# Optimization experiments

Measured on AMD Instinct MI355X. Metric: run time of the kernel, lower is better.

The kernel has to match this reference:

```python
import jax, jax.numpy as jnp
import numpy as np

N, C, H, W = 8, 128, 128, 128   # batch, emb channels, spatial
O, M, K, L = 81, 1, 3, 3        # classes, num_modes, neg_num_modes, neg MPC layers
SIGMA, BETA, NEG_SCOPE = 0.5, 0.3, 2.0
EPS = 1e-12


def _l2norm(v, axis):
    # matches F.normalize: v / max(||v||, eps)
    n = jnp.sqrt(jnp.sum(v * v, axis=axis, keepdims=True))
    return v / jnp.maximum(n, EPS)


def setup_inputs() -> dict:
    key = jax.random.key(0)
    k0, k1, k2 = jax.random.split(key, 3)
    return {
        "x": jax.random.normal(k0, (N, C, H, W), jnp.float32),
        "rep_fc_w": jax.random.normal(k1, (O * M * C,), jnp.float32) * 0.01,
        "rep_fc_b": jnp.zeros((O * M * C,), jnp.float32),
        "neg_w": jax.random.normal(k2, (K, L, C, C), jnp.float32) * 0.01,
        "neg_b": jnp.zeros((K, L, C), jnp.float32),
    }


def reference(x, rep_fc_w, rep_fc_b, neg_w, neg_b):
    # emb_module = identity; L2-normalize embeddings over channel dim
    e = _l2norm(x, axis=1)                      # (N,C,H,W)
    ehw = e.transpose(0, 2, 3, 1)               # (N,H,W,C)

    # reps = rep_fc(1.0) -> weight + bias (Linear(1, O*M*C) applied to scalar 1)
    reps = (rep_fc_w + rep_fc_b).reshape(O, M, C)
    reps = _l2norm(reps, axis=2)                # (O,1,C) unit rows

    # negative reps: K independent 3-layer MLPs (ReLU between layers)
    r = reps[:, 0, :]                           # (O,C)
    neg_list = []
    for k in range(K):
        h = r
        for l in range(L):
            h = h @ neg_w[k, l].T + neg_b[k, l]
            if l < L - 1:
                h = jax.nn.relu(h)
        neg_list.append(h)
    reps_neg = jnp.stack(neg_list, axis=1)      # (O,K,C)
    reps_neg = _l2norm(reps_neg, axis=2)

    # Both sides unit-norm -> ||e - r||^2 = 2 - 2<e,r>; compute via GEMM
    dot = jnp.einsum('nhwc,omc->nomhw', ehw, reps)        # (N,O,M,H,W)
    distances = jnp.sqrt(jax.nn.relu(2.0 - 2.0 * dot))
    dot_n = jnp.einsum('nhwc,okc->nokhw', ehw, reps_neg)  # (N,O,K,H,W)
    distances_neg = jnp.sqrt(jax.nn.relu(2.0 - 2.0 * dot_n))

    inv = 1.0 / (2.0 * SIGMA ** 2)
    probs_neg = jnp.exp(-distances_neg ** 2 * inv)
    cls_score_neg = probs_neg.max(axis=2)                 # (N,O,H,W)

    probs_ori = jnp.exp(-distances ** 2 * inv).max(axis=2)  # (N,O,H,W)

    min_neg = distances_neg.min(axis=2, keepdims=True)    # (N,O,1,H,W)
    probs = jnp.exp(-(distances + BETA * jax.nn.relu(NEG_SCOPE - min_neg)) ** 2 * inv)

    # cls_norm = True: normalize summed probs over classes
    probs_sumj = probs.sum(axis=2)                        # (N,O,H,W)
    cls_score = probs_sumj / probs_sumj.sum(axis=1, keepdims=True)

    return (cls_score, cls_score_neg, distances, distances_neg, probs_ori)
```

## Files before the change

kernel.cpp:

```cpp
#include <hip/hip_runtime.h>

#define HW 16384

typedef __attribute__((ext_vector_type(8))) short bf16x8;
typedef __attribute__((ext_vector_type(4))) float f32x4;

static constexpr size_t OFF0 = 0;
static constexpr size_t OFF1 = 10616832;
static constexpr size_t OFF2 = 21233664;
static constexpr size_t OFF3 = 31850496;
static constexpr size_t OFF4 = 63700992;

static constexpr size_t WS_R    = 0;
static constexpr size_t WS_H1   = 41472;
static constexpr size_t WS_H2   = 165888;
static constexpr size_t WS_NEGN = 290304;
static constexpr size_t WS_A    = 414720;

static __device__ __forceinline__ unsigned short f2bf(float f) {
  unsigned int u = __float_as_uint(f);
  u += 0x7fffu + ((u >> 16) & 1u);
  return (unsigned short)(u >> 16);
}

__global__ __launch_bounds__(128) void prep_first(const float* __restrict__ rw,
                                                  const float* __restrict__ rb,
                                                  const float* __restrict__ nw,
                                                  const float* __restrict__ nb,
                                                  float* __restrict__ ws_r,
                                                  float* __restrict__ ws_out) {
  const int b = blockIdx.x;
  const int k = b / 81, o = b % 81;
  const int j = threadIdx.x;
  __shared__ float hrow[128];
  __shared__ float red[2];

  float v = rw[o * 128 + j] + rb[o * 128 + j];
  float sq = v * v;
#pragma unroll
  for (int m = 1; m < 64; m <<= 1) sq += __shfl_xor(sq, m, 64);
  if ((j & 63) == 0) red[j >> 6] = sq;
  __syncthreads();
  float tot = red[0] + red[1];
  float r = v / fmaxf(sqrtf(tot), 1e-12f);
  if (k == 0) ws_r[o * 128 + j] = r;
  hrow[j] = r;
  __syncthreads();

  const float4* Wr = (const float4*)(nw + (((size_t)(k * 3 + 0)) * 128 + j) * 128);
  const float4* H  = (const float4*)hrow;
  float4 a = {0.f, 0.f, 0.f, 0.f};
#pragma unroll
  for (int q = 0; q < 32; ++q) {
    float4 wv = Wr[q]; float4 hv = H[q];
    a.x = fmaf(wv.x, hv.x, a.x); a.y = fmaf(wv.y, hv.y, a.y);
    a.z = fmaf(wv.z, hv.z, a.z); a.w = fmaf(wv.w, hv.w, a.w);
  }
  float acc = (a.x + a.y) + (a.z + a.w);
  acc += nb[(k * 3 + 0) * 128 + j];
  acc = fmaxf(acc, 0.f);
  ws_out[((size_t)(k * 81 + o)) * 128 + j] = acc;
}

__global__ __launch_bounds__(128) void prep_stage(const float* __restrict__ in,
                                                  const float* __restrict__ nw,
                                                  const float* __restrict__ nb,
                                                  float* __restrict__ out,
                                                  int l, int do_relu, int do_norm) {
  const int b = blockIdx.x;
  const int k = b / 81, o = b % 81;
  const int j = threadIdx.x;
  __shared__ float hrow[128];
  __shared__ float red[2];

  hrow[j] = in[((size_t)(k * 81 + o)) * 128 + j];
  __syncthreads();

  const float4* Wr = (const float4*)(nw + (((size_t)(k * 3 + l)) * 128 + j) * 128);
  const float4* H  = (const float4*)hrow;
  float4 a = {0.f, 0.f, 0.f, 0.f};
#pragma unroll
  for (int q = 0; q < 32; ++q) {
    float4 wv = Wr[q]; float4 hv = H[q];
    a.x = fmaf(wv.x, hv.x, a.x); a.y = fmaf(wv.y, hv.y, a.y);
    a.z = fmaf(wv.z, hv.z, a.z); a.w = fmaf(wv.w, hv.w, a.w);
  }
  float acc = (a.x + a.y) + (a.z + a.w);
  acc += nb[(k * 3 + l) * 128 + j];
  if (do_relu) acc = fmaxf(acc, 0.f);
  if (do_norm) {
    float sq = acc * acc;
#pragma unroll
    for (int m = 1; m < 64; m <<= 1) sq += __shfl_xor(sq, m, 64);
    if ((j & 63) == 0) red[j >> 6] = sq;
    __syncthreads();
    float tot = red[0] + red[1];
    acc = acc / fmaxf(sqrtf(tot), 1e-12f);
  }
  out[((size_t)(k * 81 + o)) * 128 + j] = acc;
}

__global__ __launch_bounds__(64) void prep_pack(const float* __restrict__ ws_r,
                                                const float* __restrict__ ws_negn,
                                                bf16x8* __restrict__ wsA) {
  const int mt = blockIdx.x >> 2, ks = blockIdx.x & 3;
  const int l = threadIdx.x;
  const int row = mt * 16 + (l & 15);
  const int o = row >> 2, s = row & 3;
  const int k0 = ks * 32 + (l >> 4) * 8;
  bf16x8 r = {0, 0, 0, 0, 0, 0, 0, 0};
  if (o < 81) {
    const float* src = (s == 0) ? (ws_r + (size_t)o * 128)
                                : (ws_negn + ((size_t)((s - 1) * 81 + o)) * 128);
#pragma unroll
    for (int jj = 0; jj < 8; ++jj) r[jj] = (short)f2bf(src[k0 + jj]);
  }
  wsA[(mt * 4 + ks) * 64 + l] = r;
}

__global__ __launch_bounds__(256) void main_kernel(const float* __restrict__ x,
                                                   const bf16x8* __restrict__ wsA,
                                                   float* __restrict__ out) {
  __shared__ __align__(16) char eLds[32768];
  __shared__ float ss[8][128];
  __shared__ float invn[128];

  const int b = blockIdx.x;
  const int n = b >> 7;
  const int p0 = (b & 127) << 7;
  const int t = threadIdx.x;
  const float* xb = x + ((size_t)n * 128) * HW + p0;

  {
    const int pq = (t & 31) * 4;
    const int cg = t >> 5;
    float a0 = 0.f, a1 = 0.f, a2 = 0.f, a3 = 0.f;
#pragma unroll
    for (int i = 0; i < 16; ++i) {
      const int c = i * 8 + cg;
      float4 v = *(const float4*)(xb + (size_t)c * HW + pq);
      a0 = fmaf(v.x, v.x, a0); a1 = fmaf(v.y, v.y, a1);
      a2 = fmaf(v.z, v.z, a2); a3 = fmaf(v.w, v.w, a3);
      const int c2 = c * 2;
      *(unsigned short*)(eLds + (((pq + 0) * 256 + c2) ^ (((pq + 0) & 7) << 4))) = f2bf(v.x);
      *(unsigned short*)(eLds + (((pq + 1) * 256 + c2) ^ (((pq + 1) & 7) << 4))) = f2bf(v.y);
      *(unsigned short*)(eLds + (((pq + 2) * 256 + c2) ^ (((pq + 2) & 7) << 4))) = f2bf(v.z);
      *(unsigned short*)(eLds + (((pq + 3) * 256 + c2) ^ (((pq + 3) & 7) << 4))) = f2bf(v.w);
    }
    float4 st = {a0, a1, a2, a3};
    *(float4*)&ss[cg][pq] = st;
  }
  __syncthreads();
  if (t < 128) {
    float s = 0.f;
#pragma unroll
    for (int g = 0; g < 8; ++g) s += ss[g][t];
    invn[t] = 1.f / fmaxf(sqrtf(s), 1e-12f);
  }
  __syncthreads();

  const int lane = t & 63;
  const int wv = t >> 6;
  const int og = lane >> 4;

  bf16x8 bfrag[2][4];
  float ivp[2];
#pragma unroll
  for (int u = 0; u < 2; ++u) {
    const int p = (wv * 2 + u) * 16 + (lane & 15);
#pragma unroll
    for (int ks = 0; ks < 4; ++ks) {
      const int addr = (p * 256 + ks * 64 + (lane >> 4) * 16) ^ ((p & 7) << 4);
      bfrag[u][ks] = *(const bf16x8*)(eLds + addr);
    }
    ivp[u] = invn[p];
  }

  float probs_arr[42];

#pragma unroll
  for (int mt = 0; mt < 21; ++mt) {
    bf16x8 afr[4];
#pragma unroll
    for (int ks = 0; ks < 4; ++ks) afr[ks] = wsA[(mt * 4 + ks) * 64 + lane];
    f32x4 c0 = {0.f, 0.f, 0.f, 0.f}, c1 = {0.f, 0.f, 0.f, 0.f};
#pragma unroll
    for (int ks = 0; ks < 4; ++ks) {
      c0 = __builtin_amdgcn_mfma_f32_16x16x32_bf16(afr[ks], bfrag[0][ks], c0, 0, 0, 0);
      c1 = __builtin_amdgcn_mfma_f32_16x16x32_bf16(afr[ks], bfrag[1][ks], c1, 0, 0, 0);
    }
    const int o = mt * 4 + og;
    const bool valid = (o < 81);
#pragma unroll
    for (int u = 0; u < 2; ++u) {
      const f32x4 c = u ? c1 : c0;
      const float iv = ivp[u];
      float q0 = fmaxf(2.f - 2.f * (c[0] * iv), 0.f);
      float d0 = sqrtf(q0);
      float d1 = sqrtf(fmaxf(2.f - 2.f * (c[1] * iv), 0.f));
      float d2 = sqrtf(fmaxf(2.f - 2.f * (c[2] * iv), 0.f));
      float d3 = sqrtf(fmaxf(2.f - 2.f * (c[3] * iv), 0.f));
      float dmin = fminf(d1, fminf(d2, d3));
      float pneg = __expf(-2.f * dmin * dmin);
      float pori = __expf(-2.f * q0);
      float tt = d0 + 0.3f * fmaxf(2.f - dmin, 0.f);
      float pr = __expf(-2.f * tt * tt);
      probs_arr[mt * 2 + u] = valid ? pr : 0.f;
      if (valid) {
        const int pimg = p0 + (wv * 2 + u) * 16 + (lane & 15);
        const size_t base = ((size_t)(n * 81 + o)) * HW + pimg;
        out[OFF2 + base] = d0;
        out[OFF4 + base] = pori;
        out[OFF1 + base] = pneg;
        const size_t b3 = ((size_t)((n * 81 + o) * 3)) * HW + pimg;
        out[OFF3 + b3] = d1;
        out[OFF3 + b3 + HW] = d2;
        out[OFF3 + b3 + 2 * HW] = d3;
      }
    }
  }

#pragma unroll
  for (int u = 0; u < 2; ++u) {
    float s = 0.f;
#pragma unroll
    for (int mt = 0; mt < 21; ++mt) s += probs_arr[mt * 2 + u];
    s += __shfl_xor(s, 16, 64);
    s += __shfl_xor(s, 32, 64);
    const float is = 1.f / s;
    const int pimg = p0 + (wv * 2 + u) * 16 + (lane & 15);
#pragma unroll
    for (int mt = 0; mt < 21; ++mt) {
      const int o = mt * 4 + og;
      if (o < 81) {
        const size_t base = ((size_t)(n * 81 + o)) * HW + pimg;
        out[OFF0 + base] = probs_arr[mt * 2 + u] * is;
      }
    }
  }
}

extern "C" void kernel_launch(void* const* d_in, const int* in_sizes, int n_in,
                              void* d_out, int out_size, void* d_ws, size_t ws_size,
                              hipStream_t stream) {
  const float* x  = (const float*)d_in[0];
  const float* rw = (const float*)d_in[1];
  const float* rb = (const float*)d_in[2];
  const float* nw = (const float*)d_in[3];
  const float* nb = (const float*)d_in[4];
  float* out = (float*)d_out;
  char* ws = (char*)d_ws;
  float* ws_r    = (float*)(ws + WS_R);
  float* ws_h1   = (float*)(ws + WS_H1);
  float* ws_h2   = (float*)(ws + WS_H2);
  float* ws_negn = (float*)(ws + WS_NEGN);
  bf16x8* wsA    = (bf16x8*)(ws + WS_A);

  hipLaunchKernelGGL(prep_first, dim3(243), dim3(128), 0, stream, rw, rb, nw, nb, ws_r, ws_h1);
  hipLaunchKernelGGL(prep_stage, dim3(243), dim3(128), 0, stream, ws_h1, nw, nb, ws_h2, 1, 1, 0);
  hipLaunchKernelGGL(prep_stage, dim3(243), dim3(128), 0, stream, ws_h2, nw, nb, ws_negn, 2, 0, 1);
  hipLaunchKernelGGL(prep_pack, dim3(84), dim3(64), 0, stream, ws_r, ws_negn, wsA);
  hipLaunchKernelGGL(main_kernel, dim3(1024), dim3(256), 0, stream, x, wsA, out);
}
```

Baseline: 103.5 us.

## Fuse MLP prep kernels into one and pack bf16 LDS stores in main kernel

Merges the three MLP layer kernels and the bf16 fragment-pack kernel into one prep kernel. Each block now runs all three layers in shared memory and writes the MFMA A-fragment layout directly, removing three launches and the fp32 workspace round trips. In the main kernel, each thread loads four consecutive channels and writes them as packed 8-byte bf16 stores instead of single 2-byte stores, with the LDS swizzle changed to match. The risk is a swizzle mismatch between the write and read sides, and a smaller grid of dependent work inside the single prep kernel.

```diff
diff --git a/kernel.cpp b/kernel.cpp
--- a/kernel.cpp
+++ b/kernel.cpp
@@ -11,28 +11,31 @@
 static constexpr size_t OFF3 = 31850496;
 static constexpr size_t OFF4 = 63700992;
 
-static constexpr size_t WS_R    = 0;
-static constexpr size_t WS_H1   = 41472;
-static constexpr size_t WS_H2   = 165888;
-static constexpr size_t WS_NEGN = 290304;
-static constexpr size_t WS_A    = 414720;
-
 static __device__ __forceinline__ unsigned short f2bf(float f) {
   unsigned int u = __float_as_uint(f);
   u += 0x7fffu + ((u >> 16) & 1u);
   return (unsigned short)(u >> 16);
 }
 
-__global__ __launch_bounds__(128) void prep_first(const float* __restrict__ rw,
-                                                  const float* __restrict__ rb,
-                                                  const float* __restrict__ nw,
-                                                  const float* __restrict__ nb,
-                                                  float* __restrict__ ws_r,
-                                                  float* __restrict__ ws_out) {
+static __device__ __forceinline__ void frag_write(unsigned short* wsA, int R, int j,
+                                                  unsigned short v) {
+  const int mt = R >> 4;
+  const int ks = j >> 5;
+  const int hi = (j >> 3) & 3;
+  const int jj = j & 7;
+  const int lane = hi * 16 + (R & 15);
+  wsA[((size_t)((mt * 4 + ks) * 64 + lane)) * 8 + jj] = v;
+}
+
+__global__ __launch_bounds__(128) void prep_all(const float* __restrict__ rw,
+                                                const float* __restrict__ rb,
+                                                const float* __restrict__ nw,
+                                                const float* __restrict__ nb,
+                                                unsigned short* __restrict__ wsA) {
   const int b = blockIdx.x;
   const int k = b / 81, o = b % 81;
   const int j = threadIdx.x;
-  __shared__ float hrow[128];
+  __shared__ __align__(16) float hrow[128];
   __shared__ float red[2];
 
   float v = rw[o * 128 + j] + rb[o * 128 + j];
@@ -41,81 +44,43 @@
   for (int m = 1; m < 64; m <<= 1) sq += __shfl_xor(sq, m, 64);
   if ((j & 63) == 0) red[j >> 6] = sq;
   __syncthreads();
-  float tot = red[0] + red[1];
-  float r = v / fmaxf(sqrtf(tot), 1e-12f);
-  if (k == 0) ws_r[o * 128 + j] = r;
+  const float r = v / fmaxf(sqrtf(red[0] + red[1]), 1e-12f);
+  __syncthreads();
   hrow[j] = r;
   __syncthreads();
 
-  const float4* Wr = (const float4*)(nw + (((size_t)(k * 3 + 0)) * 128 + j) * 128);
-  const float4* H  = (const float4*)hrow;
-  float4 a = {0.f, 0.f, 0.f, 0.f};
-#pragma unroll
-  for (int q = 0; q < 32; ++q) {
-    float4 wv = Wr[q]; float4 hv = H[q];
-    a.x = fmaf(wv.x, hv.x, a.x); a.y = fmaf(wv.y, hv.y, a.y);
-    a.z = fmaf(wv.z, hv.z, a.z); a.w = fmaf(wv.w, hv.w, a.w);
-  }
-  float acc = (a.x + a.y) + (a.z + a.w);
-  acc += nb[(k * 3 + 0) * 128 + j];
-  acc = fmaxf(acc, 0.f);
-  ws_out[((size_t)(k * 81 + o)) * 128 + j] = acc;
-}
-
-__global__ __launch_bounds__(128) void prep_stage(const float* __restrict__ in,
-                                                  const float* __restrict__ nw,
-                                                  const float* __restrict__ nb,
-                                                  float* __restrict__ out,
-                                                  int l, int do_relu, int do_norm) {
-  const int b = blockIdx.x;
-  const int k = b / 81, o = b % 81;
-  const int j = threadIdx.x;
-  __shared__ float hrow[128];
-  __shared__ float red[2];
-
-  hrow[j] = in[((size_t)(k * 81 + o)) * 128 + j];
-  __syncthreads();
-
-  const float4* Wr = (const float4*)(nw + (((size_t)(k * 3 + l)) * 128 + j) * 128);
-  const float4* H  = (const float4*)hrow;
-  float4 a = {0.f, 0.f, 0.f, 0.f};
-#pragma unroll
-  for (int q = 0; q < 32; ++q) {
-    float4 wv = Wr[q]; float4 hv = H[q];
-    a.x = fmaf(wv.x, hv.x, a.x); a.y = fmaf(wv.y, hv.y, a.y);
-    a.z = fmaf(wv.z, hv.z, a.z); a.w = fmaf(wv.w, hv.w, a.w);
-  }
-  float acc = (a.x + a.y) + (a.z + a.w);
-  acc += nb[(k * 3 + l) * 128 + j];
-  if (do_relu) acc = fmaxf(acc, 0.f);
-  if (do_norm) {
-    float sq = acc * acc;
-#pragma unroll
-    for (int m = 1; m < 64; m <<= 1) sq += __shfl_xor(sq, m, 64);
-    if ((j & 63) == 0) red[j >> 6] = sq;
+  float acc = 0.f;
+#pragma unroll
+  for (int l = 0; l < 3; ++l) {
+    const float4* Wr = (const float4*)(nw + (((size_t)(k * 3 + l)) * 128 + j) * 128);
+    const float4* H  = (const float4*)hrow;
+    float4 a = {0.f, 0.f, 0.f, 0.f};
+#pragma unroll
+    for (int q = 0; q < 32; ++q) {
+      float4 wv = Wr[q]; float4 hv = H[q];
+      a.x = fmaf(wv.x, hv.x, a.x); a.y = fmaf(wv.y, hv.y, a.y);
+      a.z = fmaf(wv.z, hv.z, a.z); a.w = fmaf(wv.w, hv.w, a.w);
+    }
+    acc = (a.x + a.y) + (a.z + a.w) + nb[(k * 3 + l) * 128 + j];
+    if (l < 2) acc = fmaxf(acc, 0.f);
     __syncthreads();
-    float tot = red[0] + red[1];
-    acc = acc / fmaxf(sqrtf(tot), 1e-12f);
-  }
-  out[((size_t)(k * 81 + o)) * 128 + j] = acc;
-}
-
-__global__ __launch_bounds__(64) void prep_pack(const float* __restrict__ ws_r,
-                                                const float* __restrict__ ws_negn,
-                                                bf16x8* __restrict__ wsA) {
-  const int mt = blockIdx.x >> 2, ks = blockIdx.x & 3;
-  const int l = threadIdx.x;
-  const int row = mt * 16 + (l & 15);
-  const int o = row >> 2, s = row & 3;
-  const int k0 = ks * 32 + (l >> 4) * 8;
-  bf16x8 r = {0, 0, 0, 0, 0, 0, 0, 0};
-  if (o < 81) {
-    const float* src = (s == 0) ? (ws_r + (size_t)o * 128)
-                                : (ws_negn + ((size_t)((s - 1) * 81 + o)) * 128);
-#pragma unroll
-    for (int jj = 0; jj < 8; ++jj) r[jj] = (short)f2bf(src[k0 + jj]);
-  }
-  wsA[(mt * 4 + ks) * 64 + l] = r;
+    if (l < 2) hrow[j] = acc;
+    __syncthreads();
+  }
+
+  float sq2 = acc * acc;
+#pragma unroll
+  for (int m = 1; m < 64; m <<= 1) sq2 += __shfl_xor(sq2, m, 64);
+  if ((j & 63) == 0) red[j >> 6] = sq2;
+  __syncthreads();
+  const float accn = acc / fmaxf(sqrtf(red[0] + red[1]), 1e-12f);
+
+  frag_write(wsA, o * 4 + k + 1, j, f2bf(accn));
+  if (k == 0) frag_write(wsA, o * 4, j, f2bf(r));
+  if (b == 0) {
+#pragma unroll
+    for (int R = 324; R < 336; ++R) frag_write(wsA, R, j, (unsigned short)0);
+  }
 }
 
 __global__ __launch_bounds__(256) void main_kernel(const float* __restrict__ x,
@@ -134,18 +99,32 @@
   {
     const int pq = (t & 31) * 4;
     const int cg = t >> 5;
+    const int swz = (t & 7) << 4;
     float a0 = 0.f, a1 = 0.f, a2 = 0.f, a3 = 0.f;
 #pragma unroll
-    for (int i = 0; i < 16; ++i) {
-      const int c = i * 8 + cg;
-      float4 v = *(const float4*)(xb + (size_t)c * HW + pq);
-      a0 = fmaf(v.x, v.x, a0); a1 = fmaf(v.y, v.y, a1);
-      a2 = fmaf(v.z, v.z, a2); a3 = fmaf(v.w, v.w, a3);
-      const int c2 = c * 2;
-      *(unsigned short*)(eLds + (((pq + 0) * 256 + c2) ^ (((pq + 0) & 7) << 4))) = f2bf(v.x);
-      *(unsigned short*)(eLds + (((pq + 1) * 256 + c2) ^ (((pq + 1) & 7) << 4))) = f2bf(v.y);
-      *(unsigned short*)(eLds + (((pq + 2) * 256 + c2) ^ (((pq + 2) & 7) << 4))) = f2bf(v.z);
-      *(unsigned short*)(eLds + (((pq + 3) * 256 + c2) ^ (((pq + 3) & 7) << 4))) = f2bf(v.w);
+    for (int i = 0; i < 4; ++i) {
+      const int c0 = i * 32 + cg * 4;
+      float4 v0 = *(const float4*)(xb + (size_t)(c0 + 0) * HW + pq);
+      float4 v1 = *(const float4*)(xb + (size_t)(c0 + 1) * HW + pq);
+      float4 v2 = *(const float4*)(xb + (size_t)(c0 + 2) * HW + pq);
+      float4 v3 = *(const float4*)(xb + (size_t)(c0 + 3) * HW + pq);
+      a0 = fmaf(v0.x, v0.x, fmaf(v1.x, v1.x, fmaf(v2.x, v2.x, fmaf(v3.x, v3.x, a0))));
+      a1 = fmaf(v0.y, v0.y, fmaf(v1.y, v1.y, fmaf(v2.y, v2.y, fmaf(v3.y, v3.y, a1))));
+      a2 = fmaf(v0.z, v0.z, fmaf(v1.z, v1.z, fmaf(v2.z, v2.z, fmaf(v3.z, v3.z, a2))));
+      a3 = fmaf(v0.w, v0.w, fmaf(v1.w, v1.w, fmaf(v2.w, v2.w, fmaf(v3.w, v3.w, a3))));
+      uint2 w;
+      w.x = (unsigned)f2bf(v0.x) | ((unsigned)f2bf(v1.x) << 16);
+      w.y = (unsigned)f2bf(v2.x) | ((unsigned)f2bf(v3.x) << 16);
+      *(uint2*)(eLds + (((pq + 0) * 256 + c0 * 2) ^ swz)) = w;
+      w.x = (unsigned)f2bf(v0.y) | ((unsigned)f2bf(v1.y) << 16);
+      w.y = (unsigned)f2bf(v2.y) | ((unsigned)f2bf(v3.y) << 16);
+      *(uint2*)(eLds + (((pq + 1) * 256 + c0 * 2) ^ swz)) = w;
+      w.x = (unsigned)f2bf(v0.z) | ((unsigned)f2bf(v1.z) << 16);
+      w.y = (unsigned)f2bf(v2.z) | ((unsigned)f2bf(v3.z) << 16);
+      *(uint2*)(eLds + (((pq + 2) * 256 + c0 * 2) ^ swz)) = w;
+      w.x = (unsigned)f2bf(v0.w) | ((unsigned)f2bf(v1.w) << 16);
+      w.y = (unsigned)f2bf(v2.w) | ((unsigned)f2bf(v3.w) << 16);
+      *(uint2*)(eLds + (((pq + 3) * 256 + c0 * 2) ^ swz)) = w;
     }
     float4 st = {a0, a1, a2, a3};
     *(float4*)&ss[cg][pq] = st;
@@ -168,9 +147,10 @@
 #pragma unroll
   for (int u = 0; u < 2; ++u) {
     const int p = (wv * 2 + u) * 16 + (lane & 15);
+    const int swzr = ((p >> 2) & 7) << 4;
 #pragma unroll
     for (int ks = 0; ks < 4; ++ks) {
-      const int addr = (p * 256 + ks * 64 + (lane >> 4) * 16) ^ ((p & 7) << 4);
+      const int addr = (p * 256 + ks * 64 + (lane >> 4) * 16) ^ swzr;
       bfrag[u][ks] = *(const bf16x8*)(eLds + addr);
     }
     ivp[u] = invn[p];
@@ -249,16 +229,9 @@
   const float* nw = (const float*)d_in[3];
   const float* nb = (const float*)d_in[4];
   float* out = (float*)d_out;
-  char* ws = (char*)d_ws;
-  float* ws_r    = (float*)(ws + WS_R);
-  float* ws_h1   = (float*)(ws + WS_H1);
-  float* ws_h2   = (float*)(ws + WS_H2);
-  float* ws_negn = (float*)(ws + WS_NEGN);
-  bf16x8* wsA    = (bf16x8*)(ws + WS_A);
-
-  hipLaunchKernelGGL(prep_first, dim3(243), dim3(128), 0, stream, rw, rb, nw, nb, ws_r, ws_h1);
-  hipLaunchKernelGGL(prep_stage, dim3(243), dim3(128), 0, stream, ws_h1, nw, nb, ws_h2, 1, 1, 0);
-  hipLaunchKernelGGL(prep_stage, dim3(243), dim3(128), 0, stream, ws_h2, nw, nb, ws_negn, 2, 0, 1);
-  hipLaunchKernelGGL(prep_pack, dim3(84), dim3(64), 0, stream, ws_r, ws_negn, wsA);
+  unsigned short* wsA_us = (unsigned short*)d_ws;
+  const bf16x8* wsA = (const bf16x8*)d_ws;
+
+  hipLaunchKernelGGL(prep_all, dim3(243), dim3(128), 0, stream, rw, rb, nw, nb, wsA_us);
   hipLaunchKernelGGL(main_kernel, dim3(1024), dim3(256), 0, stream, x, wsA, out);
 }
```

Measured after the change: 97.93 us. -5.4%, faster.
